# Kernel tuning notes

Measured on AMD Instinct MI355X. Metric: run time of the kernel, lower is better.

## Reference

```python
import jax, jax.numpy as jnp
import numpy as np

KERNEL_SIZE = 3  # matches init kwarg

def setup_inputs() -> dict:
    key = jax.random.key(0)
    k1, k2, k3, k4 = jax.random.split(key, 4)
    N, C, L, OUT = 32, 64, 2048, 128
    inp = jax.random.normal(k1, (N, C, L), dtype=jnp.float32)
    # adjacency-like dense matrix (tree adjacency may be sparse; dense here)
    m = jax.random.uniform(k2, (N, L, L), dtype=jnp.float32)
    W = jax.random.normal(k3, (OUT, KERNEL_SIZE * C), dtype=jnp.float32) * 0.05
    b = jax.random.normal(k4, (OUT,), dtype=jnp.float32)
    return {"input": inp, "m": m, "W": W, "b": b}

def reference(input, m, W, b):
    # propagate features over the tree adjacency kernel_size-1 times
    ys = [input]
    y = input
    for _ in range(KERNEL_SIZE - 1):
        y = jnp.matmul(y, m)          # (N, C, L) @ (N, L, L) -> (N, C, L)
        ys.append(y)
    cat = jnp.concatenate(ys, axis=1)  # (N, k*C, L)
    # 1x1 conv == channel projection
    out = jnp.einsum('oc,ncl->nol', W, cat) + b[None, :, None]
    return out
```

## Files before the change

kernel.cpp:

```cpp
#include <hip/hip_runtime.h>
#include <hip/hip_bf16.h>

#define NB   32
#define CH   64
#define LL   2048
#define OUTC 128

typedef float  f32x4  __attribute__((ext_vector_type(4)));
typedef short  s16x8  __attribute__((ext_vector_type(8)));
typedef short  s16x4  __attribute__((ext_vector_type(4)));
typedef unsigned short u16;

__device__ __forceinline__ u16 f2bf(float f) {
  unsigned int u = __builtin_bit_cast(unsigned int, f);
  u += 0x7FFFu + ((u >> 16) & 1u);
  return (u16)(u >> 16);
}

__device__ __forceinline__ s16x8 pack8c(const float* v) {
  s16x8 r;
#pragma unroll
  for (int j = 0; j < 8; j += 2) {
    __hip_bfloat162 h = __float22bfloat162_rn(make_float2(v[j], v[j + 1]));
    short2 s;
    __builtin_memcpy(&s, &h, sizeof(s));
    r[j] = s.x; r[j + 1] = s.y;
  }
  return r;
}

__device__ __forceinline__ s16x4 pack4c(const f32x4& v) {
  s16x4 r;
  __hip_bfloat162 h0 = __float22bfloat162_rn(make_float2(v[0], v[1]));
  __hip_bfloat162 h1 = __float22bfloat162_rn(make_float2(v[2], v[3]));
  short2 s0, s1;
  __builtin_memcpy(&s0, &h0, sizeof(s0));
  __builtin_memcpy(&s1, &h1, sizeof(s1));
  r[0] = s0.x; r[1] = s0.y; r[2] = s1.x; r[3] = s1.y;
  return r;
}

#define NX (NB * CH * LL)
#define NW (OUTC * 3 * CH)
__global__ __launch_bounds__(256)
void cvt_inputs(const float* __restrict__ x, const float* __restrict__ W,
                u16* __restrict__ xb, u16* __restrict__ Wb)
{
  const size_t t8 = ((size_t)blockIdx.x * 256 + threadIdx.x) * 8;
  if (t8 < NX) {
    float v[8];
    *(f32x4*)(v)     = *(const f32x4*)(x + t8);
    *(f32x4*)(v + 4) = *(const f32x4*)(x + t8 + 4);
    *(s16x8*)(xb + t8) = pack8c(v);
  } else if (t8 - NX < NW) {
    const size_t w8 = t8 - NX;
    float v[8];
    *(f32x4*)(v)     = *(const f32x4*)(W + w8);
    *(f32x4*)(v + 4) = *(const f32x4*)(W + w8 + 4);
    *(s16x8*)(Wb + w8) = pack8c(v);
  }
}

__global__ __launch_bounds__(256, 2)
void prop1_pack(const u16* __restrict__ xb, const float* __restrict__ m,
                u16* __restrict__ y1, u16* __restrict__ mP)
{
  __shared__ float smem[4][32 * 128];

  const int n    = blockIdx.x >> 4;
  const int lt   = blockIdx.x & 15;
  const int tid  = threadIdx.x;
  const int wave = tid >> 6;
  const int lane = tid & 63;
  const int l15  = lane & 15;
  const int g4   = lane >> 4;
  const int colb = lt * 128 + wave * 32;

  const float* mn   = m + (size_t)n * LL * LL + lt * 128;
  const float* gsrc = mn + (size_t)(wave * 8 + (lane >> 5)) * LL + (lane & 31) * 4;
  const u16*   ap   = xb + (size_t)n * CH * LL + (size_t)l15 * LL + g4 * 8;
  u16* q0 = mP + (((size_t)n * 64 * LL + colb + l15) * 4 + g4) * 8;
  u16* o  = y1 + (size_t)n * CH * LL + colb + l15;

  f32x4 acc[4][2];
#pragma unroll
  for (int f = 0; f < 4; ++f)
#pragma unroll
    for (int h = 0; h < 2; ++h)
#pragma unroll
      for (int r = 0; r < 4; ++r) acc[f][h][r] = 0.f;

  s16x8 aP[4], aQ[4];

#define ALOAD(R, KB)                                                          \
  { const u16* _ap = ap + (KB) * 32;                                          \
    _Pragma("unroll") for (int f = 0; f < 4; ++f)                             \
      R[f] = *(const s16x8*)(_ap + (size_t)(f * 16) * LL); }

#define GLOAD(BI, KB)                                                         \
  { float* _sb = smem[BI];                                                    \
    _Pragma("unroll") for (int i = 0; i < 4; ++i) {                           \
      const float* _g = gsrc + (size_t)((KB) * 32 + i * 2) * LL;              \
      __builtin_amdgcn_global_load_lds(                                       \
        (const __attribute__((address_space(1))) void*)_g,                    \
        (__attribute__((address_space(3))) void*)(_sb + (wave * 4 + i) * 256),\
        16, 0, 0); } }

  ALOAD(aP, 0)
  __builtin_amdgcn_sched_barrier(0);
  GLOAD(0, 0) GLOAD(1, 1) GLOAD(2, 2)
  __builtin_amdgcn_sched_barrier(0);
  asm volatile("s_waitcnt vmcnt(8)" ::: "memory");
  __builtin_amdgcn_s_barrier();
  __builtin_amdgcn_sched_barrier(0);

#define K1_STEP(KB, CUR, NXT, VN, LAST)                                       \
  {                                                                           \
    if (!(LAST)) {                                                            \
      ALOAD(NXT, ((KB) + 1 < 64 ? (KB) + 1 : 63))                             \
      __builtin_amdgcn_sched_barrier(0);                                      \
      GLOAD(((KB) + 3) & 3, ((KB) + 3 < 64 ? (KB) + 3 : 63))                  \
      __builtin_amdgcn_sched_barrier(0);                                      \
    }                                                                         \
    const float* _t = smem[(KB) & 3] + wave * 32 + l15;                       \
    float _bv0[8], _bv1[8];                                                   \
    _Pragma("unroll") for (int j = 0; j < 8; ++j) {                           \
      _bv0[j] = _t[(g4 * 8 + j) * 128];                                       \
      _bv1[j] = _t[(g4 * 8 + j) * 128 + 16];                                  \
    }                                                                         \
    s16x8 _b0 = pack8c(_bv0), _b1 = pack8c(_bv1);                             \
    u16* _q = q0 + (size_t)(KB) * 65536;                                      \
    *(s16x8*)(_q)       = _b0;                                                \
    *(s16x8*)(_q + 512) = _b1;                                                \
    _Pragma("unroll") for (int f = 0; f < 4; ++f) {                           \
      acc[f][0] = __builtin_amdgcn_mfma_f32_16x16x32_bf16(CUR[f], _b0, acc[f][0], 0, 0, 0); \
      acc[f][1] = __builtin_amdgcn_mfma_f32_16x16x32_bf16(CUR[f], _b1, acc[f][1], 0, 0, 0); \
    }                                                                         \
    if (!(LAST)) {                                                            \
      __builtin_amdgcn_sched_barrier(0);                                      \
      asm volatile("s_waitcnt vmcnt(" VN ")" ::: "memory");                   \
      __builtin_amdgcn_s_barrier();                                           \
      __builtin_amdgcn_sched_barrier(0);                                      \
    }                                                                         \
  }

  K1_STEP(0, aP, aQ, "14", false)
  K1_STEP(1, aQ, aP, "20", false)
#pragma unroll 1
  for (int kb = 2; kb < 62; kb += 2) {
    K1_STEP(kb,     aP, aQ, "22", false)
    K1_STEP(kb + 1, aQ, aP, "22", false)
  }
  K1_STEP(62, aP, aQ, "22", false)
  K1_STEP(63, aQ, aP, "0",  true)

#pragma unroll
  for (int f = 0; f < 4; ++f)
#pragma unroll
    for (int r = 0; r < 4; ++r) {
      const int row = f * 16 + g4 * 4 + r;
      o[(size_t)row * LL]      = f2bf(acc[f][0][r]);
      o[(size_t)row * LL + 16] = f2bf(acc[f][1][r]);
    }
}

__global__ __launch_bounds__(256, 2)
void prop2_proj(const u16* __restrict__ y1, const u16* __restrict__ mP,
                const u16* __restrict__ xb, const u16* __restrict__ Wb,
                const float* __restrict__ bias, float* __restrict__ out)
{
  __shared__ u16 yT[128 * 72];

  const int n    = blockIdx.x >> 4;
  const int lt   = blockIdx.x & 15;
  const int tid  = threadIdx.x;
  const int wave = tid >> 6;
  const int lane = tid & 63;
  const int l15  = lane & 15;
  const int g4   = lane >> 4;
  const int colb = lt * 128 + wave * 32;

  const u16* mq = mP + (((size_t)n * 64 * LL + colb + l15) * 4 + g4) * 8;
  const u16* ap = y1 + (size_t)n * CH * LL + (size_t)l15 * LL + g4 * 8;

  f32x4 acc[4][2];
#pragma unroll
  for (int f = 0; f < 4; ++f)
#pragma unroll
    for (int h = 0; h < 2; ++h)
#pragma unroll
      for (int r = 0; r < 4; ++r) acc[f][h][r] = 0.f;

  s16x8 bA0, bA1, bB0, bB1, aA[4], aB[4];

#define K2_LOAD(B0, B1, AV, KB)                                              \
  {                                                                          \
    const u16* _mq = mq + (size_t)(KB) * 65536;                              \
    B0 = *(const s16x8*)(_mq);                                               \
    B1 = *(const s16x8*)(_mq + 512);                                         \
    const u16* _ap = ap + (KB) * 32;                                         \
    _Pragma("unroll") for (int f = 0; f < 4; ++f)                            \
      AV[f] = *(const s16x8*)(_ap + (size_t)(f * 16) * LL);                  \
  }

#define K2_COMP(B0, B1, AV)                                                  \
  _Pragma("unroll") for (int f = 0; f < 4; ++f) {                            \
    acc[f][0] = __builtin_amdgcn_mfma_f32_16x16x32_bf16(AV[f], B0, acc[f][0], 0, 0, 0); \
    acc[f][1] = __builtin_amdgcn_mfma_f32_16x16x32_bf16(AV[f], B1, acc[f][1], 0, 0, 0); \
  }

  K2_LOAD(bA0, bA1, aA, 63)
#pragma unroll 1
  for (int kb = 63; kb >= 1; kb -= 2) {
    K2_LOAD(bB0, bB1, aB, kb - 1)
    K2_COMP(bA0, bA1, aA)
    if (kb - 2 >= 0) K2_LOAD(bA0, bA1, aA, kb - 2)
    K2_COMP(bB0, bB1, aB)
  }

#pragma unroll
  for (int f = 0; f < 4; ++f)
#pragma unroll
    for (int h = 0; h < 2; ++h) {
      const int c = wave * 32 + l15 + 16 * h;
      *(s16x4*)(&yT[c * 72 + f * 16 + g4 * 4]) = pack4c(acc[f][h]);
    }
  __syncthreads();

  f32x4 acc2[8][2];
#pragma unroll
  for (int f = 0; f < 8; ++f)
#pragma unroll
    for (int h = 0; h < 2; ++h)
#pragma unroll
      for (int r = 0; r < 4; ++r) acc2[f][h][r] = 0.f;

  const size_t cb = (size_t)n * CH * LL + colb + l15;
  const u16* xp  = xb + cb + (size_t)(g4 * 8) * LL;
  const u16* y1p = y1 + cb + (size_t)(g4 * 8) * LL;
  const u16* wq  = Wb + (size_t)l15 * 192 + g4 * 8;

#pragma unroll
  for (int kc = 0; kc < 6; ++kc) {
    const int k0 = kc * 32;
    s16x8 b0, b1;
    if (kc < 4) {
      const u16* src = (kc < 2) ? (xp + (size_t)k0 * LL)
                                : (y1p + (size_t)(k0 - 64) * LL);
#pragma unroll
      for (int j = 0; j < 8; ++j) {
        b0[j] = (short)src[(size_t)j * LL];
        b1[j] = (short)src[(size_t)j * LL + 16];
      }
    } else {
      const int rb = (kc - 4) * 32 + g4 * 8;
      b0 = *(const s16x8*)(&yT[(wave * 32 + l15) * 72 + rb]);
      b1 = *(const s16x8*)(&yT[(wave * 32 + l15 + 16) * 72 + rb]);
    }
#pragma unroll
    for (int f = 0; f < 8; ++f) {
      s16x8 af = *(const s16x8*)(wq + (size_t)(f * 16) * 192 + k0);
      acc2[f][0] = __builtin_amdgcn_mfma_f32_16x16x32_bf16(af, b0, acc2[f][0], 0, 0, 0);
      acc2[f][1] = __builtin_amdgcn_mfma_f32_16x16x32_bf16(af, b1, acc2[f][1], 0, 0, 0);
    }
  }

  float* op = out + (size_t)n * OUTC * LL + colb + l15;
#pragma unroll
  for (int f = 0; f < 8; ++f)
#pragma unroll
    for (int r = 0; r < 4; ++r) {
      const int row = f * 16 + g4 * 4 + r;
      op[(size_t)row * LL]      = acc2[f][0][r] + bias[row];
      op[(size_t)row * LL + 16] = acc2[f][1][r] + bias[row];
    }
}

extern "C" void kernel_launch(void* const* d_in, const int* in_sizes, int n_in,
                              void* d_out, int out_size, void* d_ws, size_t ws_size,
                              hipStream_t stream)
{
  const float* x = (const float*)d_in[0];
  const float* m = (const float*)d_in[1];
  const float* W = (const float*)d_in[2];
  const float* b = (const float*)d_in[3];
  float* out = (float*)d_out;

  u16* y1 = (u16*)d_ws;
  u16* xb = y1 + (size_t)NB * CH * LL;
  u16* Wb = xb + (size_t)NB * CH * LL;
  u16* mP = (u16*)((char*)d_ws + (25u << 20));

  cvt_inputs<<<dim3(2060), dim3(256), 0, stream>>>(x, W, xb, Wb);
  prop1_pack<<<dim3(NB * 16), dim3(256), 0, stream>>>(xb, m, y1, mP);
  prop2_proj<<<dim3(NB * 16), dim3(256), 0, stream>>>(y1, mP, xb, Wb, b, out);
}
```

Baseline: 270.4 us.

## Shrink prop1 LDS ring to three stages and raise occupancy to three blocks

Cuts the prop1 shared-memory ring buffer from four to three stages, dropping LDS per block from 64KB to 48KB. With that, both kernels can declare launch bounds of three blocks per CU. The prefetch distance falls from 3 to 2 k-blocks, and the loop is unrolled by six so buffer indices stay compile-time constants, with the vmcnt wait counts retuned to match. The aim is to hide memory latency through more resident waves rather than deeper per-block prefetch, at the cost of tighter register budgets and less lookahead within each block.

After: 271.3 us. No clear change (+0.3%).

```diff
diff --git a/kernel.cpp b/kernel.cpp
--- a/kernel.cpp
+++ b/kernel.cpp
@@ -61,11 +61,11 @@
   }
 }
 
-__global__ __launch_bounds__(256, 2)
+__global__ __launch_bounds__(256, 3)
 void prop1_pack(const u16* __restrict__ xb, const float* __restrict__ m,
                 u16* __restrict__ y1, u16* __restrict__ mP)
 {
-  __shared__ float smem[4][32 * 128];
+  __shared__ float smem[3][32 * 128];
 
   const int n    = blockIdx.x >> 4;
   const int lt   = blockIdx.x & 15;
@@ -108,21 +108,23 @@
 
   ALOAD(aP, 0)
   __builtin_amdgcn_sched_barrier(0);
-  GLOAD(0, 0) GLOAD(1, 1) GLOAD(2, 2)
+  GLOAD(0, 0) GLOAD(1, 1)
   __builtin_amdgcn_sched_barrier(0);
-  asm volatile("s_waitcnt vmcnt(8)" ::: "memory");
+  asm volatile("s_waitcnt vmcnt(4)" ::: "memory");
   __builtin_amdgcn_s_barrier();
   __builtin_amdgcn_sched_barrier(0);
 
-#define K1_STEP(KB, CUR, NXT, VN, LAST)                                       \
+#define K1_STEP(KB, CUR, NXT, GI, BI, VN, DOA, DOG, DOBAR)                    \
   {                                                                           \
-    if (!(LAST)) {                                                            \
-      ALOAD(NXT, ((KB) + 1 < 64 ? (KB) + 1 : 63))                             \
+    if (DOA) {                                                                \
+      ALOAD(NXT, (KB) + 1)                                                    \
       __builtin_amdgcn_sched_barrier(0);                                      \
-      GLOAD(((KB) + 3) & 3, ((KB) + 3 < 64 ? (KB) + 3 : 63))                  \
+    }                                                                         \
+    if (DOG) {                                                                \
+      GLOAD(GI, (KB) + 2)                                                     \
       __builtin_amdgcn_sched_barrier(0);                                      \
     }                                                                         \
-    const float* _t = smem[(KB) & 3] + wave * 32 + l15;                       \
+    const float* _t = smem[BI] + wave * 32 + l15;                             \
     float _bv0[8], _bv1[8];                                                   \
     _Pragma("unroll") for (int j = 0; j < 8; ++j) {                           \
       _bv0[j] = _t[(g4 * 8 + j) * 128];                                       \
@@ -136,7 +138,7 @@
       acc[f][0] = __builtin_amdgcn_mfma_f32_16x16x32_bf16(CUR[f], _b0, acc[f][0], 0, 0, 0); \
       acc[f][1] = __builtin_amdgcn_mfma_f32_16x16x32_bf16(CUR[f], _b1, acc[f][1], 0, 0, 0); \
     }                                                                         \
-    if (!(LAST)) {                                                            \
+    if (DOBAR) {                                                              \
       __builtin_amdgcn_sched_barrier(0);                                      \
       asm volatile("s_waitcnt vmcnt(" VN ")" ::: "memory");                   \
       __builtin_amdgcn_s_barrier();                                           \
@@ -144,15 +146,19 @@
     }                                                                         \
   }
 
-  K1_STEP(0, aP, aQ, "14", false)
-  K1_STEP(1, aQ, aP, "20", false)
+  K1_STEP(0, aP, aQ, 2, 0, "10", 1, 1, 1)
 #pragma unroll 1
-  for (int kb = 2; kb < 62; kb += 2) {
-    K1_STEP(kb,     aP, aQ, "22", false)
-    K1_STEP(kb + 1, aQ, aP, "22", false)
-  }
-  K1_STEP(62, aP, aQ, "22", false)
-  K1_STEP(63, aQ, aP, "0",  true)
+  for (int kb = 1; kb <= 55; kb += 6) {
+    K1_STEP(kb,     aQ, aP, 0, 1, "12", 1, 1, 1)
+    K1_STEP(kb + 1, aP, aQ, 1, 2, "12", 1, 1, 1)
+    K1_STEP(kb + 2, aQ, aP, 2, 0, "12", 1, 1, 1)
+    K1_STEP(kb + 3, aP, aQ, 0, 1, "12", 1, 1, 1)
+    K1_STEP(kb + 4, aQ, aP, 1, 2, "12", 1, 1, 1)
+    K1_STEP(kb + 5, aP, aQ, 2, 0, "12", 1, 1, 1)
+  }
+  K1_STEP(61, aQ, aP, 0, 1, "12", 1, 1, 1)
+  K1_STEP(62, aP, aQ, 0, 2, "8",  1, 0, 1)
+  K1_STEP(63, aQ, aP, 0, 0, "0",  0, 0, 0)
 
 #pragma unroll
   for (int f = 0; f < 4; ++f)
@@ -164,7 +170,7 @@
     }
 }
 
-__global__ __launch_bounds__(256, 2)
+__global__ __launch_bounds__(256, 3)
 void prop2_proj(const u16* __restrict__ y1, const u16* __restrict__ mP,
                 const u16* __restrict__ xb, const u16* __restrict__ Wb,
                 const float* __restrict__ bias, float* __restrict__ out)
```
